# Optimization experiments

Hardware: AMD Instinct MI355X
Metric: run time of the kernel (lower is better)

Reference implementation:

```python
import jax, jax.numpy as jnp
import numpy as np

B, S, D = 2, 1024, 768
NH = 12
DH = D // NH
HID = 1536
G, EPG = 4, 2
E = G * EPG
TEMP = 1.0
LN_EPS = 1e-5


def setup_inputs() -> dict:
    key = jax.random.key(0)
    ks = jax.random.split(key, 8)
    s = 0.02
    return {
        "x": jax.random.normal(ks[0], (B, S, D), jnp.float32),
        "ln1_w": jnp.ones((D,), jnp.float32),
        "ln1_b": jnp.zeros((D,), jnp.float32),
        "in_proj_w": jax.random.normal(ks[1], (3 * D, D), jnp.float32) * s,
        "in_proj_b": jnp.zeros((3 * D,), jnp.float32),
        "out_proj_w": jax.random.normal(ks[2], (D, D), jnp.float32) * s,
        "out_proj_b": jnp.zeros((D,), jnp.float32),
        "ln2_w": jnp.ones((D,), jnp.float32),
        "ln2_b": jnp.zeros((D,), jnp.float32),
        "Wg": jax.random.normal(ks[3], (D, G), jnp.float32) * s,
        "bg": jnp.zeros((G,), jnp.float32),
        "We": jax.random.normal(ks[4], (G, D, EPG), jnp.float32) * s,
        "be": jnp.zeros((G, EPG), jnp.float32),
        "W1": jax.random.normal(ks[5], (E, D, HID), jnp.float32) * s,
        "b1": jnp.zeros((E, HID), jnp.float32),
        "W2": jax.random.normal(ks[6], (E, HID, D), jnp.float32) * s,
        "b2": jnp.zeros((E, D), jnp.float32),
    }


def _ln(x, w, b):
    m = x.mean(-1, keepdims=True)
    v = x.var(-1, keepdims=True)
    return (x - m) / jnp.sqrt(v + LN_EPS) * w + b


def _mha(h, wqkv, bqkv, wo, bo):
    qkv = h @ wqkv.T + bqkv                       # [B,S,3D]
    q, k, v = jnp.split(qkv, 3, axis=-1)
    q = q.reshape(B, S, NH, DH)
    k = k.reshape(B, S, NH, DH)
    v = v.reshape(B, S, NH, DH)
    scale = 1.0 / np.sqrt(DH).astype(np.float32)
    att = jnp.einsum("bqhd,bkhd->bhqk", q, k) * scale
    p = jax.nn.softmax(att, axis=-1)
    o = jnp.einsum("bhqk,bkhd->bqhd", p, v).reshape(B, S, D)
    return o @ wo.T + bo


def _moe(h, Wg, bg, We, be, W1, b1, W2, b2):
    hf = h.reshape(-1, D)                         # [N,D] tokens
    # level-1: group router (temperature softmax, top-1)
    gp = jax.nn.softmax((hf @ Wg + bg) / TEMP, axis=-1)          # [N,G]
    g = jnp.argmax(gp, axis=-1)                                   # [N]
    pg = jnp.take_along_axis(gp, g[:, None], axis=1)[:, 0]        # [N]
    # level-2: within-group expert router
    el = jnp.einsum("nd,gde->nge", hf, We) + be                   # [N,G,EPG]
    ep = jax.nn.softmax(el / TEMP, axis=-1)
    ep_g = jnp.take_along_axis(ep, g[:, None, None], axis=1)[:, 0, :]  # [N,EPG]
    e = jnp.argmax(ep_g, axis=-1)                                 # [N]
    pe = jnp.take_along_axis(ep_g, e[:, None], axis=1)[:, 0]      # [N]
    flat = g * EPG + e                                            # flat expert id [N]
    combine = jax.nn.one_hot(flat, E, dtype=hf.dtype) * (pg * pe)[:, None]  # [N,E]
    # dense expert compute (reference form of dispatch/grouped-GEMM/combine)
    hid = jax.nn.gelu(jnp.einsum("nd,edh->enh", hf, W1) + b1[:, None, :])   # [E,N,HID]
    y = jnp.einsum("enh,ehd->end", hid, W2) + b2[:, None, :]                # [E,N,D]
    out = jnp.einsum("ne,end->nd", combine, y)                              # [N,D]
    return out.reshape(h.shape)


def reference(x, ln1_w, ln1_b, in_proj_w, in_proj_b, out_proj_w, out_proj_b,
              ln2_w, ln2_b, Wg, bg, We, be, W1, b1, W2, b2):
    a = _mha(_ln(x, ln1_w, ln1_b), in_proj_w, in_proj_b, out_proj_w, out_proj_b)
    x = x + a  # dropout p=0.0 -> identity
    m = _moe(_ln(x, ln2_w, ln2_b), Wg, bg, We, be, W1, b1, W2, b2)
    return x + m
```

## Files before the change

### kernel.cpp

```cpp
#include <hip/hip_runtime.h>
#include <stdint.h>

#define B_ 2
#define S_ 1024
#define D_ 768
#define NH_ 12
#define DH_ 64
#define HID_ 1536
#define G_ 4
#define EPG_ 2
#define E_ 8
#define NTOK (B_*S_)
#define NGRP (B_*NH_*16)

typedef unsigned short u16;
typedef __bf16 bf16x8 __attribute__((ext_vector_type(8)));
typedef float f32x4 __attribute__((ext_vector_type(4)));
typedef u16 u16x4 __attribute__((ext_vector_type(4)));
typedef u16 u16x8 __attribute__((ext_vector_type(8)));

struct BfPair { u16 hi, lo; };

__device__ __forceinline__ u16 f2bf(float f){
  unsigned u = __builtin_bit_cast(unsigned, f);
  u += 0x7FFFu + ((u >> 16) & 1u);
  return (u16)(u >> 16);
}
__device__ __forceinline__ float bf2f(u16 h){
  unsigned u = ((unsigned)h) << 16;
  return __builtin_bit_cast(float, u);
}
__device__ __forceinline__ BfPair split_bf(float v){
  BfPair p;
  p.hi = f2bf(v);
  p.lo = f2bf(v - bf2f(p.hi));
  return p;
}
__device__ __forceinline__ float gelu_tanh(float x){
  float t = 0.7978845608028654f * (x + 0.044715f * x * x * x);
  float e = __expf(2.f * t);
  float th = 1.f - 2.f / (e + 1.f);
  return 0.5f * x * (1.f + th);
}
__device__ __forceinline__ void gload_lds16(const void* g, void* l){
  __builtin_amdgcn_global_load_lds(
      (const __attribute__((address_space(1))) void*)g,
      (__attribute__((address_space(3))) void*)l, 16, 0, 0);
}

__global__ __launch_bounds__(256) void k_prep(
    const float* __restrict__ in_proj_w, const float* __restrict__ out_proj_w,
    const float* __restrict__ W1, const float* __restrict__ W2,
    u16* __restrict__ inpTh, u16* __restrict__ inpTl,
    u16* __restrict__ outpTh, u16* __restrict__ outpTl,
    u16* __restrict__ W1t, u16* __restrict__ W2t){
  __shared__ float tile[32][33];
  int bid = blockIdx.x, t = threadIdx.x;
  if (bid < 2304){
    const float* src; u16 *dh, *dl; int i;
    if (bid < 1728){ src = in_proj_w; dh = inpTh; dl = inpTl; i = bid * 256 + t; }
    else           { src = out_proj_w; dh = outpTh; dl = outpTl; i = (bid - 1728) * 256 + t; }
    float4 v = ((const float4*)src)[i];
    u16x4 oh, ol;
    BfPair p0 = split_bf(v.x), p1 = split_bf(v.y), p2 = split_bf(v.z), p3 = split_bf(v.w);
    oh.x = p0.hi; ol.x = p0.lo; oh.y = p1.hi; ol.y = p1.lo;
    oh.z = p2.hi; ol.z = p2.lo; oh.w = p3.hi; ol.w = p3.lo;
    ((u16x4*)dh)[i] = oh;
    ((u16x4*)dl)[i] = ol;
  } else {
    const float* src; u16* dst; int R, C, cx, cy, e;
    if (bid < 11520){
      int r = bid - 2304; e = r / 1152; r %= 1152;
      R = D_; C = HID_; cx = r % 48; cy = r / 48;
      src = W1; dst = W1t;
    } else {
      int r = bid - 11520; e = r / 1152; r %= 1152;
      R = HID_; C = D_; cx = r % 24; cy = r / 24;
      src = W2; dst = W2t;
    }
    const float* s = src + (size_t)e * R * C;
    u16* d = dst + (size_t)e * R * C;
    int c0 = cx * 32, r0 = cy * 32;
    int tx = t & 31, ty = t >> 5;
    #pragma unroll
    for (int i = 0; i < 32; i += 8)
      tile[ty + i][tx] = s[(size_t)(r0 + ty + i) * C + c0 + tx];
    __syncthreads();
    #pragma unroll
    for (int i = 0; i < 32; i += 8)
      d[(size_t)(c0 + ty + i) * R + r0 + tx] = f2bf(tile[tx][ty + i]);
  }
}

__global__ void k_transpose_v(const u16* __restrict__ qh, const u16* __restrict__ ql,
                              u16* __restrict__ vth, u16* __restrict__ vtl){
  __shared__ u16 th[32][34], tl[32][34];
  int bh = blockIdx.z, b = bh / NH_, h = bh % NH_;
  int d0 = blockIdx.x * 32, s0 = blockIdx.y * 32;
  #pragma unroll
  for (int i = 0; i < 32; i += 8){
    size_t src = (size_t)(b * S_ + s0 + threadIdx.y + i) * (3 * D_) + 2 * D_ + h * DH_ + d0 + threadIdx.x;
    th[threadIdx.y + i][threadIdx.x] = qh[src];
    tl[threadIdx.y + i][threadIdx.x] = ql[src];
  }
  __syncthreads();
  #pragma unroll
  for (int i = 0; i < 32; i += 8){
    size_t dst = ((size_t)bh * DH_ + d0 + threadIdx.y + i) * S_ + s0 + threadIdx.x;
    vth[dst] = th[threadIdx.x][threadIdx.y + i];
    vtl[dst] = tl[threadIdx.x][threadIdx.y + i];
  }
}

__global__ __launch_bounds__(256) void k_layernorm(
    const float* __restrict__ x, const float* __restrict__ w, const float* __restrict__ b,
    u16* __restrict__ oh, u16* __restrict__ ol, float* __restrict__ of){
  int row = blockIdx.x;
  const float* xr = x + (size_t)row * D_;
  int t = threadIdx.x;
  float v0 = xr[t], v1 = xr[t + 256], v2 = xr[t + 512];
  float s = v0 + v1 + v2;
  float sq = v0 * v0 + v1 * v1 + v2 * v2;
  #pragma unroll
  for (int m = 1; m < 64; m <<= 1){ s += __shfl_xor(s, m); sq += __shfl_xor(sq, m); }
  __shared__ float ls[4], lq[4];
  int wid = t >> 6;
  if ((t & 63) == 0){ ls[wid] = s; lq[wid] = sq; }
  __syncthreads();
  s = ls[0] + ls[1] + ls[2] + ls[3];
  sq = lq[0] + lq[1] + lq[2] + lq[3];
  float mean = s * (1.f / D_);
  float var = sq * (1.f / D_) - mean * mean;
  float rstd = rsqrtf(var + 1e-5f);
  #pragma unroll
  for (int i = 0; i < 3; i++){
    int dcol = t + i * 256;
    float v = (i == 0 ? v0 : (i == 1 ? v1 : v2));
    float y = (v - mean) * rstd * w[dcol] + b[dcol];
    BfPair p = split_bf(y);
    oh[(size_t)row * D_ + dcol] = p.hi;
    if (ol) ol[(size_t)row * D_ + dcol] = p.lo;
    if (of) of[(size_t)row * D_ + dcol] = y;
  }
}

template<int EPI>
__global__ __launch_bounds__(256) void k_gemm3(
    const u16* __restrict__ Ah, const u16* __restrict__ Al,
    const u16* __restrict__ Bh, const u16* __restrict__ Bl,
    const float* __restrict__ bias, const float* __restrict__ resid,
    u16* __restrict__ outh, u16* __restrict__ outl, float* __restrict__ outf,
    int M, int N, int K){
  __shared__ alignas(16) u16 Ash[2][64 * 32];
  __shared__ alignas(16) u16 Asl[2][64 * 32];
  __shared__ alignas(16) u16 Bsh[2][64 * 32];
  __shared__ alignas(16) u16 Bsl[2][64 * 32];
  int m0 = blockIdx.x * 64, n0 = blockIdx.y * 64;
  int tid = threadIdx.x, w = tid >> 6, l = tid & 63;
  int wr = w >> 1, wc = w & 1;
  f32x4 acc[2][2];
  #pragma unroll
  for (int i = 0; i < 2; i++)
    #pragma unroll
    for (int j = 0; j < 2; j++) acc[i][j] = f32x4{0.f, 0.f, 0.f, 0.f};
  int srow = w * 16 + (l >> 2);
  int scol = 8 * ((l & 3) ^ ((l >> 2) & 3));
  const u16* gAh = Ah + (size_t)(m0 + srow) * K + scol;
  const u16* gAl = Al + (size_t)(m0 + srow) * K + scol;
  const u16* gBh = Bh + (size_t)(n0 + srow) * K + scol;
  const u16* gBl = Bl + (size_t)(n0 + srow) * K + scol;
  int dOff = (w * 16) * 32;
  auto STAGE = [&](int buf, int k0){
    gload_lds16(gAh + k0, &Ash[buf][dOff]);
    gload_lds16(gAl + k0, &Asl[buf][dOff]);
    gload_lds16(gBh + k0, &Bsh[buf][dOff]);
    gload_lds16(gBl + k0, &Bsl[buf][dOff]);
  };
  STAGE(0, 0);
  __syncthreads();
  int nk = K / 32;
  int ca = (l >> 4) ^ (l & 3);
  int ai = (wr * 32 + (l & 15)) * 32 + 8 * ca;
  int bi = (wc * 32 + (l & 15)) * 32 + 8 * ca;
  for (int t = 0; t < nk; t++){
    int cur = t & 1;
    if (t + 1 < nk) STAGE(cur ^ 1, (t + 1) * 32);
    bf16x8 afh[2], afl[2], bfh[2], bfl[2];
    #pragma unroll
    for (int mi = 0; mi < 2; mi++){
      afh[mi] = *(const bf16x8*)&Ash[cur][ai + mi * 16 * 32];
      afl[mi] = *(const bf16x8*)&Asl[cur][ai + mi * 16 * 32];
    }
    #pragma unroll
    for (int ni = 0; ni < 2; ni++){
      bfh[ni] = *(const bf16x8*)&Bsh[cur][bi + ni * 16 * 32];
      bfl[ni] = *(const bf16x8*)&Bsl[cur][bi + ni * 16 * 32];
    }
    #pragma unroll
    for (int mi = 0; mi < 2; mi++)
      #pragma unroll
      for (int ni = 0; ni < 2; ni++){
        acc[mi][ni] = __builtin_amdgcn_mfma_f32_16x16x32_bf16(afh[mi], bfh[ni], acc[mi][ni], 0, 0, 0);
        acc[mi][ni] = __builtin_amdgcn_mfma_f32_16x16x32_bf16(afh[mi], bfl[ni], acc[mi][ni], 0, 0, 0);
        acc[mi][ni] = __builtin_amdgcn_mfma_f32_16x16x32_bf16(afl[mi], bfh[ni], acc[mi][ni], 0, 0, 0);
      }
    __syncthreads();
  }
  int r4 = (l >> 4) * 4, cc = l & 15;
  #pragma unroll
  for (int mi = 0; mi < 2; mi++){
    #pragma unroll
    for (int ni = 0; ni < 2; ni++){
      int col = n0 + wc * 32 + ni * 16 + cc;
      float bv = bias ? bias[col] : 0.f;
      #pragma unroll
      for (int r = 0; r < 4; r++){
        int row = m0 + wr * 32 + mi * 16 + r4 + r;
        float v = acc[mi][ni][r] + bv;
        if (EPI == 0){
          BfPair p = split_bf(v);
          outh[(size_t)row * N + col] = p.hi;
          outl[(size_t)row * N + col] = p.lo;
        } else {
          outf[(size_t)row * N + col] = v + resid[(size_t)row * N + col];
        }
      }
    }
  }
}

__global__ __launch_bounds__(256) void k_attn3(
    const u16* __restrict__ qkvh, const u16* __restrict__ qkvl,
    const u16* __restrict__ vth, const u16* __restrict__ vtl,
    float* __restrict__ po0, float* __restrict__ po1,
    float* __restrict__ pm, float* __restrict__ plsum){
  __shared__ alignas(16) u16 Ksh[2][32 * 64];
  __shared__ alignas(16) u16 Ksl[2][32 * 64];
  __shared__ alignas(16) u16 Vsh[2][64 * 32];
  __shared__ alignas(16) u16 Vsl[2][64 * 32];
  __shared__ alignas(16) u16 Ph[4 * 16 * 32];
  __shared__ alignas(16) u16 Pl[4 * 16 * 32];
  int bh = blockIdx.x, qb = blockIdx.y, ks = blockIdx.z;
  int b = bh / NH_, h = bh % NH_;
  int g = bh * 16 + qb;
  int tid = threadIdx.x, w = tid >> 6, l = tid & 63;
  int q0 = qb * 64 + w * 16;
  const int RS = 3 * D_;
  size_t qoff = (size_t)(b * S_ + q0 + (l & 15)) * RS + h * DH_ + 8 * (l >> 4);
  bf16x8 aqh[2], aql[2];
  aqh[0] = *(const bf16x8*)(qkvh + qoff); aqh[1] = *(const bf16x8*)(qkvh + qoff + 32);
  aql[0] = *(const bf16x8*)(qkvl + qoff); aql[1] = *(const bf16x8*)(qkvl + qoff + 32);
  f32x4 oacc[4];
  #pragma unroll
  for (int i = 0; i < 4; i++) oacc[i] = f32x4{0.f, 0.f, 0.f, 0.f};
  float mrun[4], lrun[4];
  #pragma unroll
  for (int r = 0; r < 4; r++){ mrun[r] = -1e30f; lrun[r] = 0.f; }

  size_t koff = (size_t)(b * S_ + w * 8 + (l >> 3)) * RS + D_ + h * DH_ + 8 * ((l & 7) ^ (l >> 3));
  const u16* Kgh = qkvh + koff;
  const u16* Kgl = qkvl + koff;
  size_t voff = ((size_t)bh * DH_ + w * 16 + (l >> 2)) * S_ + 8 * ((l & 3) ^ ((l >> 2) & 3));
  const u16* Vgh = vth + voff;
  const u16* Vgl = vtl + voff;
  int wdst = w * 512;

  auto STAGE = [&](int buf, int akt){
    gload_lds16(Kgh + (size_t)(akt * 32) * RS, &Ksh[buf][wdst]);
    gload_lds16(Kgl + (size_t)(akt * 32) * RS, &Ksl[buf][wdst]);
    gload_lds16(Vgh + akt * 32, &Vsh[buf][wdst]);
    gload_lds16(Vgl + akt * 32, &Vsl[buf][wdst]);
  };
  int kt0 = ks * 16;
  STAGE(0, kt0);
  __syncthreads();

  int ck0 = (l >> 4) ^ (l & 7);
  int ck1 = ck0 ^ 4;
  int cv = (l >> 4) ^ (l & 3);

  for (int kt = 0; kt < 16; kt++){
    int cur = kt & 1;
    if (kt + 1 < 16) STAGE(cur ^ 1, kt0 + kt + 1);
    f32x4 st[2];
    #pragma unroll
    for (int nt = 0; nt < 2; nt++){
      int rbase = (nt * 16 + (l & 15)) * 64;
      bf16x8 kh0 = *(const bf16x8*)&Ksh[cur][rbase + 8 * ck0];
      bf16x8 kh1 = *(const bf16x8*)&Ksh[cur][rbase + 8 * ck1];
      bf16x8 kl0 = *(const bf16x8*)&Ksl[cur][rbase + 8 * ck0];
      bf16x8 kl1 = *(const bf16x8*)&Ksl[cur][rbase + 8 * ck1];
      f32x4 c = f32x4{0.f, 0.f, 0.f, 0.f};
      c = __builtin_amdgcn_mfma_f32_16x16x32_bf16(aqh[0], kh0, c, 0, 0, 0);
      c = __builtin_amdgcn_mfma_f32_16x16x32_bf16(aqh[1], kh1, c, 0, 0, 0);
      c = __builtin_amdgcn_mfma_f32_16x16x32_bf16(aqh[0], kl0, c, 0, 0, 0);
      c = __builtin_amdgcn_mfma_f32_16x16x32_bf16(aqh[1], kl1, c, 0, 0, 0);
      c = __builtin_amdgcn_mfma_f32_16x16x32_bf16(aql[0], kh0, c, 0, 0, 0);
      c = __builtin_amdgcn_mfma_f32_16x16x32_bf16(aql[1], kh1, c, 0, 0, 0);
      st[nt] = c;
    }
    float mnew[4], alpha[4];
    #pragma unroll
    for (int r = 0; r < 4; r++){
      float mx = fmaxf(st[0][r], st[1][r]) * 0.125f;
      #pragma unroll
      for (int m = 1; m < 16; m <<= 1) mx = fmaxf(mx, __shfl_xor(mx, m));
      mnew[r] = fmaxf(mrun[r], mx);
      alpha[r] = __expf(mrun[r] - mnew[r]);
      mrun[r] = mnew[r];
    }
    float pv[2][4];
    #pragma unroll
    for (int r = 0; r < 4; r++){
      float srow = 0.f;
      #pragma unroll
      for (int nt = 0; nt < 2; nt++){
        float v = __expf(st[nt][r] * 0.125f - mnew[r]);
        pv[nt][r] = v; srow += v;
      }
      #pragma unroll
      for (int m = 1; m < 16; m <<= 1) srow += __shfl_xor(srow, m);
      lrun[r] = lrun[r] * alpha[r] + srow;
    }
    #pragma unroll
    for (int nt = 0; nt < 2; nt++)
      #pragma unroll
      for (int r = 0; r < 4; r++){
        BfPair p = split_bf(pv[nt][r]);
        int q = (l >> 4) * 4 + r;
        int col = nt * 16 + (l & 15);
        int pidx = wdst + q * 32 + (((col >> 3) ^ (q & 3)) << 3) + (col & 7);
        Ph[pidx] = p.hi;
        Pl[pidx] = p.lo;
      }
    asm volatile("s_waitcnt lgkmcnt(0)" ::: "memory");
    __builtin_amdgcn_sched_barrier(0);
    #pragma unroll
    for (int t4 = 0; t4 < 4; t4++)
      #pragma unroll
      for (int r = 0; r < 4; r++) oacc[t4][r] *= alpha[r];
    int pb = wdst + (l & 15) * 32 + 8 * cv;
    bf16x8 aph = *(const bf16x8*)&Ph[pb];
    bf16x8 apl = *(const bf16x8*)&Pl[pb];
    #pragma unroll
    for (int dt = 0; dt < 4; dt++){
      int vb = (dt * 16 + (l & 15)) * 32 + 8 * cv;
      bf16x8 bvh = *(const bf16x8*)&Vsh[cur][vb];
      bf16x8 bvl = *(const bf16x8*)&Vsl[cur][vb];
      oacc[dt] = __builtin_amdgcn_mfma_f32_16x16x32_bf16(aph, bvh, oacc[dt], 0, 0, 0);
      oacc[dt] = __builtin_amdgcn_mfma_f32_16x16x32_bf16(aph, bvl, oacc[dt], 0, 0, 0);
      oacc[dt] = __builtin_amdgcn_mfma_f32_16x16x32_bf16(apl, bvh, oacc[dt], 0, 0, 0);
    }
    __syncthreads();
  }
  float* po = ks ? po1 : po0;
  #pragma unroll
  for (int dt = 0; dt < 4; dt++)
    #pragma unroll
    for (int r = 0; r < 4; r++){
      int qloc = w * 16 + (l >> 4) * 4 + r;
      int d = dt * 16 + (l & 15);
      po[((size_t)(g * 64 + qloc)) * 64 + d] = oacc[dt][r];
    }
  if ((l & 15) == 0){
    #pragma unroll
    for (int r = 0; r < 4; r++){
      int qloc = w * 16 + (l >> 4) * 4 + r;
      pm[(ks * NGRP + g) * 64 + qloc] = mrun[r];
      plsum[(ks * NGRP + g) * 64 + qloc] = lrun[r];
    }
  }
}

__global__ __launch_bounds__(256) void k_attn_merge(
    const float* __restrict__ po0, const float* __restrict__ po1,
    const float* __restrict__ pm, const float* __restrict__ plsum,
    u16* __restrict__ oh, u16* __restrict__ ol){
  int bh = blockIdx.x, qb = blockIdx.y;
  int b = bh / NH_, h = bh % NH_;
  int g = bh * 16 + qb;
  int t = threadIdx.x;
  int q = t >> 2, d0 = (t & 3) * 16;
  float m0 = pm[g * 64 + q],      m1 = pm[NGRP * 64 + g * 64 + q];
  float l0 = plsum[g * 64 + q],   l1 = plsum[NGRP * 64 + g * 64 + q];
  float M = fmaxf(m0, m1);
  float a0 = __expf(m0 - M), a1 = __expf(m1 - M);
  float rcp = 1.f / (l0 * a0 + l1 * a1);
  size_t base = ((size_t)(g * 64 + q)) * 64 + d0;
  size_t orow = (size_t)(b * S_ + qb * 64 + q) * D_ + h * DH_ + d0;
  #pragma unroll
  for (int j = 0; j < 16; j++){
    float v = (po0[base + j] * a0 + po1[base + j] * a1) * rcp;
    BfPair p = split_bf(v);
    oh[orow + j] = p.hi;
    ol[orow + j] = p.lo;
  }
}

__global__ __launch_bounds__(256) void k_router(
    const float* __restrict__ h2f, const float* __restrict__ Wg, const float* __restrict__ bg,
    const float* __restrict__ We, const float* __restrict__ be,
    int* __restrict__ flat, float* __restrict__ pc){
  int w = threadIdx.x >> 6, l = threadIdx.x & 63;
  int n = blockIdx.x * 4 + w;
  const float* hr = h2f + (size_t)n * D_;
  float pl[4] = {0.f, 0.f, 0.f, 0.f};
  for (int d = l; d < D_; d += 64){
    float hv = hr[d];
    float4 wg = *(const float4*)&Wg[d * 4];
    pl[0] += hv * wg.x; pl[1] += hv * wg.y; pl[2] += hv * wg.z; pl[3] += hv * wg.w;
  }
  #pragma unroll
  for (int m = 1; m < 64; m <<= 1)
    #pragma unroll
    for (int g = 0; g < 4; g++) pl[g] += __shfl_xor(pl[g], m);
  float lg[4];
  #pragma unroll
  for (int g = 0; g < 4; g++) lg[g] = pl[g] + bg[g];
  int gi = 0; float gm = lg[0];
  #pragma unroll
  for (int g = 1; g < 4; g++) if (lg[g] > gm){ gm = lg[g]; gi = g; }
  float gs = 0.f;
  #pragma unroll
  for (int g = 0; g < 4; g++) gs += expf(lg[g] - gm);
  float pg = 1.f / gs;
  float e0 = 0.f, e1 = 0.f;
  for (int d = l; d < D_; d += 64){
    float hv = hr[d];
    float2 we = *(const float2*)&We[((size_t)gi * D_ + d) * 2];
    e0 += hv * we.x; e1 += hv * we.y;
  }
  #pragma unroll
  for (int m = 1; m < 64; m <<= 1){ e0 += __shfl_xor(e0, m); e1 += __shfl_xor(e1, m); }
  e0 += be[gi * 2]; e1 += be[gi * 2 + 1];
  int ei; float pe;
  if (e1 > e0){ ei = 1; pe = 1.f / (1.f + expf(e0 - e1)); }
  else        { ei = 0; pe = 1.f / (1.f + expf(e1 - e0)); }
  if (l == 0){
    flat[n] = gi * 2 + ei;
    pc[n] = pg * pe;
  }
}

__global__ __launch_bounds__(1024) void k_bucket(
    const int* __restrict__ flat, int* __restrict__ moeI, int* __restrict__ order){
  __shared__ int cnt[E_], off[E_], cur[E_];
  int t = threadIdx.x;
  if (t < E_){ cnt[t] = 0; cur[t] = 0; }
  __syncthreads();
  int n0 = t, n1 = t + 1024;
  int f0 = flat[n0], f1 = flat[n1];
  atomicAdd(&cnt[f0], 1);
  atomicAdd(&cnt[f1], 1);
  __syncthreads();
  if (t == 0){
    int s = 0;
    for (int e = 0; e < E_; e++){
      off[e] = s; moeI[16 + e] = s; moeI[e] = cnt[e]; s += cnt[e];
    }
  }
  __syncthreads();
  int p0 = atomicAdd(&cur[f0], 1);
  order[off[f0] + p0] = n0;
  int p1 = atomicAdd(&cur[f1], 1);
  order[off[f1] + p1] = n1;
}

__global__ __launch_bounds__(256) void k_moe_gemm1(
    const u16* __restrict__ h2, const u16* __restrict__ W1t, const float* __restrict__ b1,
    const int* __restrict__ order, const int* __restrict__ moeI, u16* __restrict__ hid){
  int e = blockIdx.x, mt = blockIdx.y, nt = blockIdx.z;
  int cnt = moeI[e];
  if (mt * 64 >= cnt) return;
  int off = moeI[16 + e];
  __shared__ alignas(16) u16 As[2][64 * 64];
  __shared__ alignas(16) u16 Bs[2][64 * 64];
  int tid = threadIdx.x, w = tid >> 6, l = tid & 63;
  int wr = w >> 1, wc = w & 1;
  f32x4 acc[2][2];
  #pragma unroll
  for (int i = 0; i < 2; i++)
    #pragma unroll
    for (int j = 0; j < 2; j++) acc[i][j] = f32x4{0.f, 0.f, 0.f, 0.f};
  int r0 = w * 16 + (l >> 3);
  int sch = 8 * ((l & 7) ^ (l >> 3));
  int tokA0 = order[off + min(mt * 64 + r0, cnt - 1)];
  int tokA1 = order[off + min(mt * 64 + r0 + 8, cnt - 1)];
  const u16* gA0 = h2 + (size_t)tokA0 * D_ + sch;
  const u16* gA1 = h2 + (size_t)tokA1 * D_ + sch;
  const u16* gB0 = W1t + (size_t)e * HID_ * D_ + (size_t)(nt * 64 + r0) * D_ + sch;
  const u16* gB1 = gB0 + (size_t)8 * D_;
  int d0 = (w * 16) * 64, d1 = (w * 16 + 8) * 64;
  auto STAGE = [&](int buf, int k0){
    gload_lds16(gA0 + k0, &As[buf][d0]);
    gload_lds16(gA1 + k0, &As[buf][d1]);
    gload_lds16(gB0 + k0, &Bs[buf][d0]);
    gload_lds16(gB1 + k0, &Bs[buf][d1]);
  };
  STAGE(0, 0);
  __syncthreads();
  int c0 = (l >> 4) ^ (l & 7);
  int c1 = ((l >> 4) + 4) ^ (l & 7);
  const int nk = D_ / 64;
  for (int t = 0; t < nk; t++){
    int cur = t & 1;
    if (t + 1 < nk) STAGE(cur ^ 1, (t + 1) * 64);
    bf16x8 af[2][2], bfr[2][2];
    #pragma unroll
    for (int mi = 0; mi < 2; mi++){
      int rbase = (wr * 32 + mi * 16 + (l & 15)) * 64;
      af[mi][0] = *(const bf16x8*)&As[cur][rbase + 8 * c0];
      af[mi][1] = *(const bf16x8*)&As[cur][rbase + 8 * c1];
    }
    #pragma unroll
    for (int ni = 0; ni < 2; ni++){
      int rbase = (wc * 32 + ni * 16 + (l & 15)) * 64;
      bfr[ni][0] = *(const bf16x8*)&Bs[cur][rbase + 8 * c0];
      bfr[ni][1] = *(const bf16x8*)&Bs[cur][rbase + 8 * c1];
    }
    #pragma unroll
    for (int mi = 0; mi < 2; mi++)
      #pragma unroll
      for (int ni = 0; ni < 2; ni++){
        acc[mi][ni] = __builtin_amdgcn_mfma_f32_16x16x32_bf16(af[mi][0], bfr[ni][0], acc[mi][ni], 0, 0, 0);
        acc[mi][ni] = __builtin_amdgcn_mfma_f32_16x16x32_bf16(af[mi][1], bfr[ni][1], acc[mi][ni], 0, 0, 0);
      }
    __syncthreads();
  }
  int r4 = (l >> 4) * 4, cc = l & 15;
  #pragma unroll
  for (int mi = 0; mi < 2; mi++){
    #pragma unroll
    for (int ni = 0; ni < 2; ni++){
      int col = nt * 64 + wc * 32 + ni * 16 + cc;
      float bv = b1[e * HID_ + col];
      #pragma unroll
      for (int r = 0; r < 4; r++){
        int rowl = mt * 64 + wr * 32 + mi * 16 + r4 + r;
        if (rowl < cnt){
          float v = gelu_tanh(acc[mi][ni][r] + bv);
          hid[(size_t)(off + rowl) * HID_ + col] = f2bf(v);
        }
      }
    }
  }
}

__global__ __launch_bounds__(256) void k_moe_gemm2(
    const u16* __restrict__ hid, const u16* __restrict__ W2t, const float* __restrict__ b2,
    const int* __restrict__ order, const int* __restrict__ moeI,
    const float* __restrict__ pc, const float* __restrict__ x2, float* __restrict__ out){
  int e = blockIdx.x, mt = blockIdx.y, nt = blockIdx.z;
  int cnt = moeI[e];
  if (mt * 64 >= cnt) return;
  int off = moeI[16 + e];
  __shared__ alignas(16) u16 As[2][64 * 64];
  __shared__ alignas(16) u16 Bs[2][64 * 64];
  int tid = threadIdx.x, w = tid >> 6, l = tid & 63;
  int wr = w >> 1, wc = w & 1;
  f32x4 acc[2][2];
  #pragma unroll
  for (int i = 0; i < 2; i++)
    #pragma unroll
    for (int j = 0; j < 2; j++) acc[i][j] = f32x4{0.f, 0.f, 0.f, 0.f};
  int r0 = w * 16 + (l >> 3);
  int sch = 8 * ((l & 7) ^ (l >> 3));
  int ar0 = off + min(mt * 64 + r0, cnt - 1);
  int ar1 = off + min(mt * 64 + r0 + 8, cnt - 1);
  const u16* gA0 = hid + (size_t)ar0 * HID_ + sch;
  const u16* gA1 = hid + (size_t)ar1 * HID_ + sch;
  const u16* gB0 = W2t + (size_t)e * D_ * HID_ + (size_t)(nt * 64 + r0) * HID_ + sch;
  const u16* gB1 = gB0 + (size_t)8 * HID_;
  int d0 = (w * 16) * 64, d1 = (w * 16 + 8) * 64;
  auto STAGE = [&](int buf, int k0){
    gload_lds16(gA0 + k0, &As[buf][d0]);
    gload_lds16(gA1 + k0, &As[buf][d1]);
    gload_lds16(gB0 + k0, &Bs[buf][d0]);
    gload_lds16(gB1 + k0, &Bs[buf][d1]);
  };
  STAGE(0, 0);
  __syncthreads();
  int c0 = (l >> 4) ^ (l & 7);
  int c1 = ((l >> 4) + 4) ^ (l & 7);
  const int nk = HID_ / 64;
  for (int t = 0; t < nk; t++){
    int cur = t & 1;
    if (t + 1 < nk) STAGE(cur ^ 1, (t + 1) * 64);
    bf16x8 af[2][2], bfr[2][2];
    #pragma unroll
    for (int mi = 0; mi < 2; mi++){
      int rbase = (wr * 32 + mi * 16 + (l & 15)) * 64;
      af[mi][0] = *(const bf16x8*)&As[cur][rbase + 8 * c0];
      af[mi][1] = *(const bf16x8*)&As[cur][rbase + 8 * c1];
    }
    #pragma unroll
    for (int ni = 0; ni < 2; ni++){
      int rbase = (wc * 32 + ni * 16 + (l & 15)) * 64;
      bfr[ni][0] = *(const bf16x8*)&Bs[cur][rbase + 8 * c0];
      bfr[ni][1] = *(const bf16x8*)&Bs[cur][rbase + 8 * c1];
    }
    #pragma unroll
    for (int mi = 0; mi < 2; mi++)
      #pragma unroll
      for (int ni = 0; ni < 2; ni++){
        acc[mi][ni] = __builtin_amdgcn_mfma_f32_16x16x32_bf16(af[mi][0], bfr[ni][0], acc[mi][ni], 0, 0, 0);
        acc[mi][ni] = __builtin_amdgcn_mfma_f32_16x16x32_bf16(af[mi][1], bfr[ni][1], acc[mi][ni], 0, 0, 0);
      }
    __syncthreads();
  }
  int r4 = (l >> 4) * 4, cc = l & 15;
  #pragma unroll
  for (int mi = 0; mi < 2; mi++){
    #pragma unroll
    for (int r = 0; r < 4; r++){
      int rowl = mt * 64 + wr * 32 + mi * 16 + r4 + r;
      if (rowl < cnt){
        int tok = order[off + rowl];
        float pv = pc[tok];
        #pragma unroll
        for (int ni = 0; ni < 2; ni++){
          int col = nt * 64 + wc * 32 + ni * 16 + cc;
          float v = acc[mi][ni][r] + b2[e * D_ + col];
          out[(size_t)tok * D_ + col] = x2[(size_t)tok * D_ + col] + pv * v;
        }
      }
    }
  }
}

extern "C" void kernel_launch(void* const* d_in, const int* in_sizes, int n_in,
                              void* d_out, int out_size, void* d_ws, size_t ws_size,
                              hipStream_t stream){
  const float* x         = (const float*)d_in[0];
  const float* ln1_w     = (const float*)d_in[1];
  const float* ln1_b     = (const float*)d_in[2];
  const float* in_proj_w = (const float*)d_in[3];
  const float* in_proj_b = (const float*)d_in[4];
  const float* out_proj_w= (const float*)d_in[5];
  const float* out_proj_b= (const float*)d_in[6];
  const float* ln2_w     = (const float*)d_in[7];
  const float* ln2_b     = (const float*)d_in[8];
  const float* Wg        = (const float*)d_in[9];
  const float* bg        = (const float*)d_in[10];
  const float* We        = (const float*)d_in[11];
  const float* be        = (const float*)d_in[12];
  const float* W1        = (const float*)d_in[13];
  const float* b1        = (const float*)d_in[14];
  const float* W2        = (const float*)d_in[15];
  const float* b2        = (const float*)d_in[16];
  float* out = (float*)d_out;

  char* ws = (char*)d_ws;
  size_t off = 0;
  auto alloc = [&](size_t bytes) -> char* {
    char* p = ws + off;
    off += (bytes + 255) & ~(size_t)255;
    return p;
  };
  u16*   inpTh = (u16*)  alloc((size_t)3 * D_ * D_ * 2);
  u16*   inpTl = (u16*)  alloc((size_t)3 * D_ * D_ * 2);
  u16*   outpTh= (u16*)  alloc((size_t)D_ * D_ * 2);
  u16*   outpTl= (u16*)  alloc((size_t)D_ * D_ * 2);
  u16*   W1t  = (u16*)  alloc((size_t)E_ * HID_ * D_ * 2);
  u16*   W2t  = (u16*)  alloc((size_t)E_ * D_ * HID_ * 2);
  u16*   qkvh = (u16*)  alloc((size_t)NTOK * 3 * D_ * 2);
  u16*   qkvl = (u16*)  alloc((size_t)NTOK * 3 * D_ * 2);
  u16*   h1h  = (u16*)  alloc((size_t)NTOK * D_ * 2);
  u16*   h1l  = (u16*)  alloc((size_t)NTOK * D_ * 2);
  u16*   vth  = (u16*)  alloc((size_t)B_ * NH_ * DH_ * S_ * 2);
  u16*   vtl  = (u16*)  alloc((size_t)B_ * NH_ * DH_ * S_ * 2);
  float* x2   = (float*)alloc((size_t)NTOK * D_ * 4);
  u16*   h2   = (u16*)  alloc((size_t)NTOK * D_ * 2);
  int*   flat = (int*)  alloc(NTOK * 4);
  float* pc   = (float*)alloc(NTOK * 4);
  int*   order= (int*)  alloc(NTOK * 4);
  int*   moeI = (int*)  alloc(32 * 4);
  float* po0  = (float*)h1h;
  float* po1  = (float*)inpTh;
  float* pmArr= (float*)((char*)inpTh + 6291456);
  float* plArr= (float*)((char*)inpTh + 6291456 + 196608);
  u16*   attnh= qkvh;
  u16*   attnl= qkvl;
  float* h2f  = (float*)qkvh;
  u16*   hid  = (u16*)qkvl;

  k_prep<<<dim3(20736), dim3(256), 0, stream>>>(
      in_proj_w, out_proj_w, W1, W2, inpTh, inpTl, outpTh, outpTl, W1t, W2t);
  k_layernorm<<<dim3(NTOK), dim3(256), 0, stream>>>(x, ln1_w, ln1_b, h1h, h1l, (float*)nullptr);
  k_gemm3<0><<<dim3(NTOK / 64, 3 * D_ / 64), dim3(256), 0, stream>>>(
      h1h, h1l, inpTh, inpTl, in_proj_b, nullptr, qkvh, qkvl, nullptr, NTOK, 3 * D_, D_);
  k_transpose_v<<<dim3(DH_ / 32, S_ / 32, B_ * NH_), dim3(32, 8), 0, stream>>>(qkvh, qkvl, vth, vtl);
  k_attn3<<<dim3(B_ * NH_, S_ / 64, 2), dim3(256), 0, stream>>>(
      qkvh, qkvl, vth, vtl, po0, po1, pmArr, plArr);
  k_attn_merge<<<dim3(B_ * NH_, S_ / 64), dim3(256), 0, stream>>>(
      po0, po1, pmArr, plArr, attnh, attnl);
  k_gemm3<1><<<dim3(NTOK / 64, D_ / 64), dim3(256), 0, stream>>>(
      attnh, attnl, outpTh, outpTl, out_proj_b, x, nullptr, nullptr, x2, NTOK, D_, D_);
  k_layernorm<<<dim3(NTOK), dim3(256), 0, stream>>>(x2, ln2_w, ln2_b, h2, (u16*)nullptr, h2f);
  k_router<<<dim3(NTOK / 4), dim3(256), 0, stream>>>(h2f, Wg, bg, We, be, flat, pc);
  k_bucket<<<dim3(1), dim3(1024), 0, stream>>>(flat, moeI, order);
  k_moe_gemm1<<<dim3(E_, NTOK / 64, HID_ / 64), dim3(256), 0, stream>>>(h2, W1t, b1, order, moeI, hid);
  k_moe_gemm2<<<dim3(E_, NTOK / 64, D_ / 64), dim3(256), 0, stream>>>(hid, W2t, b2, order, moeI, pc, x2, out);
}
```

Before: 217.5 us.

## Compute transposed S tile in attention to keep P in registers via shuffles

Swaps the MFMA operand order so each lane holds scores for a single query row, which reduces the row max/sum reductions to two cross-lane shuffles each. The probabilities are then rearranged into the A-operand layout with ds_bpermute-style shuffles instead of a round trip through shared memory, and the P LDS buffers plus their waitcnt barrier are dropped. In exchange there are many more shuffle instructions per tile, plus extra shuffles to broadcast alpha, and the register-level fragment mapping must be exactly right.

```diff
diff --git a/kernel.cpp b/kernel.cpp
--- a/kernel.cpp
+++ b/kernel.cpp
@@ -14,10 +14,11 @@
 #define NGRP (B_*NH_*16)
 
 typedef unsigned short u16;
+typedef unsigned int u32;
 typedef __bf16 bf16x8 __attribute__((ext_vector_type(8)));
 typedef float f32x4 __attribute__((ext_vector_type(4)));
 typedef u16 u16x4 __attribute__((ext_vector_type(4)));
-typedef u16 u16x8 __attribute__((ext_vector_type(8)));
+typedef u32 u32x4 __attribute__((ext_vector_type(4)));
 
 struct BfPair { u16 hi, lo; };
 
@@ -238,8 +239,6 @@
   __shared__ alignas(16) u16 Ksl[2][32 * 64];
   __shared__ alignas(16) u16 Vsh[2][64 * 32];
   __shared__ alignas(16) u16 Vsl[2][64 * 32];
-  __shared__ alignas(16) u16 Ph[4 * 16 * 32];
-  __shared__ alignas(16) u16 Pl[4 * 16 * 32];
   int bh = blockIdx.x, qb = blockIdx.y, ks = blockIdx.z;
   int b = bh / NH_, h = bh % NH_;
   int g = bh * 16 + qb;
@@ -253,9 +252,7 @@
   f32x4 oacc[4];
   #pragma unroll
   for (int i = 0; i < 4; i++) oacc[i] = f32x4{0.f, 0.f, 0.f, 0.f};
-  float mrun[4], lrun[4];
-  #pragma unroll
-  for (int r = 0; r < 4; r++){ mrun[r] = -1e30f; lrun[r] = 0.f; }
+  float mrun = -1e30f, lrun = 0.f;
 
   size_t koff = (size_t)(b * S_ + w * 8 + (l >> 3)) * RS + D_ + h * DH_ + 8 * ((l & 7) ^ (l >> 3));
   const u16* Kgh = qkvh + koff;
@@ -278,6 +275,9 @@
   int ck0 = (l >> 4) ^ (l & 7);
   int ck1 = ck0 ^ 4;
   int cv = (l >> 4) ^ (l & 3);
+  int s1 = (l & 15) | ((l & 16) << 1);
+  int s2 = s1 + 16;
+  bool up = (l & 32) != 0;
 
   for (int kt = 0; kt < 16; kt++){
     int cur = kt & 1;
@@ -291,65 +291,64 @@
       bf16x8 kl0 = *(const bf16x8*)&Ksl[cur][rbase + 8 * ck0];
       bf16x8 kl1 = *(const bf16x8*)&Ksl[cur][rbase + 8 * ck1];
       f32x4 c = f32x4{0.f, 0.f, 0.f, 0.f};
-      c = __builtin_amdgcn_mfma_f32_16x16x32_bf16(aqh[0], kh0, c, 0, 0, 0);
-      c = __builtin_amdgcn_mfma_f32_16x16x32_bf16(aqh[1], kh1, c, 0, 0, 0);
-      c = __builtin_amdgcn_mfma_f32_16x16x32_bf16(aqh[0], kl0, c, 0, 0, 0);
-      c = __builtin_amdgcn_mfma_f32_16x16x32_bf16(aqh[1], kl1, c, 0, 0, 0);
-      c = __builtin_amdgcn_mfma_f32_16x16x32_bf16(aql[0], kh0, c, 0, 0, 0);
-      c = __builtin_amdgcn_mfma_f32_16x16x32_bf16(aql[1], kh1, c, 0, 0, 0);
+      c = __builtin_amdgcn_mfma_f32_16x16x32_bf16(kh0, aqh[0], c, 0, 0, 0);
+      c = __builtin_amdgcn_mfma_f32_16x16x32_bf16(kh1, aqh[1], c, 0, 0, 0);
+      c = __builtin_amdgcn_mfma_f32_16x16x32_bf16(kh0, aql[0], c, 0, 0, 0);
+      c = __builtin_amdgcn_mfma_f32_16x16x32_bf16(kh1, aql[1], c, 0, 0, 0);
+      c = __builtin_amdgcn_mfma_f32_16x16x32_bf16(kl0, aqh[0], c, 0, 0, 0);
+      c = __builtin_amdgcn_mfma_f32_16x16x32_bf16(kl1, aqh[1], c, 0, 0, 0);
       st[nt] = c;
     }
-    float mnew[4], alpha[4];
+    float mx = fmaxf(fmaxf(fmaxf(st[0][0], st[0][1]), fmaxf(st[0][2], st[0][3])),
+                     fmaxf(fmaxf(st[1][0], st[1][1]), fmaxf(st[1][2], st[1][3])));
+    mx = fmaxf(mx, __shfl_xor(mx, 16));
+    mx = fmaxf(mx, __shfl_xor(mx, 32));
+    mx *= 0.125f;
+    float mnew = fmaxf(mrun, mx);
+    float alpha = __expf(mrun - mnew);
+    mrun = mnew;
+    float p[8]; float sum = 0.f;
+    #pragma unroll
+    for (int j = 0; j < 8; j++){
+      p[j] = __expf(st[j >> 2][j & 3] * 0.125f - mnew);
+      sum += p[j];
+    }
+    sum += __shfl_xor(sum, 16);
+    sum += __shfl_xor(sum, 32);
+    lrun = lrun * alpha + sum;
+    u32 pkh[4], pkl[4];
+    #pragma unroll
+    for (int i = 0; i < 4; i++){
+      BfPair a = split_bf(p[2 * i]), bb = split_bf(p[2 * i + 1]);
+      pkh[i] = (u32)a.hi | ((u32)bb.hi << 16);
+      pkl[i] = (u32)a.lo | ((u32)bb.lo << 16);
+    }
+    u32 ah0 = __shfl((int)pkh[0], s1), ah1 = __shfl((int)pkh[1], s1);
+    u32 ah2 = __shfl((int)pkh[2], s1), ah3 = __shfl((int)pkh[3], s1);
+    u32 bh0 = __shfl((int)pkh[0], s2), bh1 = __shfl((int)pkh[1], s2);
+    u32 bh2 = __shfl((int)pkh[2], s2), bh3 = __shfl((int)pkh[3], s2);
+    u32 al0 = __shfl((int)pkl[0], s1), al1 = __shfl((int)pkl[1], s1);
+    u32 al2 = __shfl((int)pkl[2], s1), al3 = __shfl((int)pkl[3], s1);
+    u32 bl0 = __shfl((int)pkl[0], s2), bl1 = __shfl((int)pkl[1], s2);
+    u32 bl2 = __shfl((int)pkl[2], s2), bl3 = __shfl((int)pkl[3], s2);
+    u32x4 fh, fl;
+    fh.x = up ? ah2 : ah0; fh.y = up ? ah3 : ah1; fh.z = up ? bh2 : bh0; fh.w = up ? bh3 : bh1;
+    fl.x = up ? al2 : al0; fl.y = up ? al3 : al1; fl.z = up ? bl2 : bl0; fl.w = up ? bl3 : bl1;
+    bf16x8 pa_h = __builtin_bit_cast(bf16x8, fh);
+    bf16x8 pa_l = __builtin_bit_cast(bf16x8, fl);
     #pragma unroll
     for (int r = 0; r < 4; r++){
-      float mx = fmaxf(st[0][r], st[1][r]) * 0.125f;
-      #pragma unroll
-      for (int m = 1; m < 16; m <<= 1) mx = fmaxf(mx, __shfl_xor(mx, m));
-      mnew[r] = fmaxf(mrun[r], mx);
-      alpha[r] = __expf(mrun[r] - mnew[r]);
-      mrun[r] = mnew[r];
-    }
-    float pv[2][4];
-    #pragma unroll
-    for (int r = 0; r < 4; r++){
-      float srow = 0.f;
-      #pragma unroll
-      for (int nt = 0; nt < 2; nt++){
-        float v = __expf(st[nt][r] * 0.125f - mnew[r]);
-        pv[nt][r] = v; srow += v;
-      }
-      #pragma unroll
-      for (int m = 1; m < 16; m <<= 1) srow += __shfl_xor(srow, m);
-      lrun[r] = lrun[r] * alpha[r] + srow;
-    }
-    #pragma unroll
-    for (int nt = 0; nt < 2; nt++)
-      #pragma unroll
-      for (int r = 0; r < 4; r++){
-        BfPair p = split_bf(pv[nt][r]);
-        int q = (l >> 4) * 4 + r;
-        int col = nt * 16 + (l & 15);
-        int pidx = wdst + q * 32 + (((col >> 3) ^ (q & 3)) << 3) + (col & 7);
-        Ph[pidx] = p.hi;
-        Pl[pidx] = p.lo;
-      }
-    asm volatile("s_waitcnt lgkmcnt(0)" ::: "memory");
-    __builtin_amdgcn_sched_barrier(0);
-    #pragma unroll
-    for (int t4 = 0; t4 < 4; t4++)
-      #pragma unroll
-      for (int r = 0; r < 4; r++) oacc[t4][r] *= alpha[r];
-    int pb = wdst + (l & 15) * 32 + 8 * cv;
-    bf16x8 aph = *(const bf16x8*)&Ph[pb];
-    bf16x8 apl = *(const bf16x8*)&Pl[pb];
+      float ar = __shfl(alpha, (l & 48) | (((l >> 4) << 2) + r));
+      oacc[0][r] *= ar; oacc[1][r] *= ar; oacc[2][r] *= ar; oacc[3][r] *= ar;
+    }
     #pragma unroll
     for (int dt = 0; dt < 4; dt++){
       int vb = (dt * 16 + (l & 15)) * 32 + 8 * cv;
       bf16x8 bvh = *(const bf16x8*)&Vsh[cur][vb];
       bf16x8 bvl = *(const bf16x8*)&Vsl[cur][vb];
-      oacc[dt] = __builtin_amdgcn_mfma_f32_16x16x32_bf16(aph, bvh, oacc[dt], 0, 0, 0);
-      oacc[dt] = __builtin_amdgcn_mfma_f32_16x16x32_bf16(aph, bvl, oacc[dt], 0, 0, 0);
-      oacc[dt] = __builtin_amdgcn_mfma_f32_16x16x32_bf16(apl, bvh, oacc[dt], 0, 0, 0);
+      oacc[dt] = __builtin_amdgcn_mfma_f32_16x16x32_bf16(pa_h, bvh, oacc[dt], 0, 0, 0);
+      oacc[dt] = __builtin_amdgcn_mfma_f32_16x16x32_bf16(pa_h, bvl, oacc[dt], 0, 0, 0);
+      oacc[dt] = __builtin_amdgcn_mfma_f32_16x16x32_bf16(pa_l, bvh, oacc[dt], 0, 0, 0);
     }
     __syncthreads();
   }
@@ -362,13 +361,9 @@
       int d = dt * 16 + (l & 15);
       po[((size_t)(g * 64 + qloc)) * 64 + d] = oacc[dt][r];
     }
-  if ((l & 15) == 0){
-    #pragma unroll
-    for (int r = 0; r < 4; r++){
-      int qloc = w * 16 + (l >> 4) * 4 + r;
-      pm[(ks * NGRP + g) * 64 + qloc] = mrun[r];
-      plsum[(ks * NGRP + g) * 64 + qloc] = lrun[r];
-    }
+  if (l < 16){
+    pm[(ks * NGRP + g) * 64 + w * 16 + l] = mrun;
+    plsum[(ks * NGRP + g) * 64 + w * 16 + l] = lrun;
   }
 }
 
```

New measurement: 207.1 us. -4.8%, faster.
